# Kernel optimization log

Hardware: AMD Instinct MI355X
Metric: run time of the kernel (lower is better)

The kernel has to match this reference:

```python
import jax, jax.numpy as jnp
import numpy as np


def _conv1d_same(seq, w, b):
    # seq: (N, 1, C), w: (1, 1, K) odd K, bias (1,). SAME padding, stride 1.
    k = w.shape[-1]
    p = (k - 1) // 2
    out = jax.lax.conv_general_dilated(
        seq, w, window_strides=(1,), padding=[(p, p)],
        dimension_numbers=("NCH", "OIH", "NCH"))
    return out + b[None, :, None]


def setup_inputs() -> dict:
    key = jax.random.key(0)
    k1, k2, k3 = jax.random.split(key, 3)
    N, C, H, W = 32, 512, 32, 32
    x = jax.random.normal(k1, (N, C, H, W), dtype=jnp.float32)
    wq = jax.random.normal(k2, (1, 1, 5), dtype=jnp.float32) * 0.2
    bq = jax.random.normal(k3, (1,), dtype=jnp.float32) * 0.1
    return {"x": x, "wq": wq, "bq": bq}


def reference(x, wq, bq):
    N, C, H, W = x.shape
    # Global average pool over spatial dims -> (N, 1, C)
    gap = jnp.mean(x, axis=(2, 3)).reshape(N, 1, C)
    # NOTE: original module applies conv_q to BOTH query and key (conv_k unused)
    query = jax.nn.sigmoid(_conv1d_same(gap, wq, bq))          # (N, 1, C)
    key_t = jnp.transpose(query, (0, 2, 1))                    # (N, C, 1)
    # Outer product key @ query -> (N, C, C), softmax over flattened C*C
    qk = jnp.einsum("nci,nij->ncj", key_t, query)              # (N, C, C)
    qk = jax.nn.softmax(qk.reshape(N, C * C), axis=-1).reshape(N, C, C)
    # value: (N, H*W, C)
    value = jnp.transpose(x, (0, 2, 3, 1)).reshape(N, H * W, C)
    att = jnp.einsum("npc,ncd->npd", value, qk)                # (N, HW, C)
    att = jnp.transpose(att, (0, 2, 1)).reshape(N, C, H, W)
    return x * att
```

## Files before the change

kernel.cpp:

```cpp
#include <hip/hip_runtime.h>
#include <math.h>

#define NB 32
#define CC 512
#define HW 1024
#define NJ 10

__device__ float g_gap[NB * CC];

__device__ __forceinline__ float wave_reduce(float s) {
#pragma unroll
  for (int off = 32; off; off >>= 1) s += __shfl_down(s, off, 64);
  return s;
}

__global__ __launch_bounds__(256) void k_gap(const float* __restrict__ x) {
  int wv = threadIdx.x >> 6, lane = threadIdx.x & 63;
  int r0 = blockIdx.x * 16;
#pragma unroll
  for (int it = 0; it < 4; ++it) {
    int row = r0 + wv * 4 + it;
    const float4* xp = (const float4*)x + (size_t)row * 256;
    float s = 0.f;
#pragma unroll
    for (int k = 0; k < 4; ++k) {
      float4 v = xp[lane + 64 * k];
      s += v.x + v.y + v.z + v.w;
    }
    s = wave_reduce(s);
    if (lane == 0) g_gap[row] = s * (1.0f / 1024.0f);
  }
}

__global__ __launch_bounds__(512) void k_fused(const float* __restrict__ x,
                                               const float* __restrict__ wq,
                                               const float* __restrict__ bq,
                                               float* __restrict__ out) {
  int n = blockIdx.x >> 4, pblk = blockIdx.x & 15;
  int t = threadIdx.x;
  int cg = t >> 4, pg = t & 15;
  int wv = t >> 6, lane = t & 63;

  __shared__ float qs[CC];
  __shared__ float wred[8][NJ];
  __shared__ float4 sred[8][16][NJ + 1];
  __shared__ float4 sfin[16][NJ + 1];
  __shared__ float invZ_sh;

  const float cj[NJ] = {1.f, 1.f, 0.5f, 1.f / 6.f, 1.f / 24.f, 1.f / 120.f,
                        1.f / 720.f, 1.f / 5040.f, 1.f / 40320.f, 1.f / 362880.f};

  float4 xv[16];
  const float4* x4 = (const float4*)x;
  size_t base = (size_t)(n * CC + cg * 16) * 256 + (size_t)pblk * 16 + pg;
#pragma unroll
  for (int i = 0; i < 16; ++i) xv[i] = x4[base + (size_t)i * 256];

  {
    int c = t;
    const float* g = g_gap + n * CC;
    float z = bq[0];
#pragma unroll
    for (int k = 0; k < 5; ++k) {
      int idx = c + k - 2;
      float gv = (idx >= 0 && idx < CC) ? g[idx] : 0.f;
      z = fmaf(gv, wq[k], z);
    }
    float qv = 1.f / (1.f + expf(-z));
    qs[c] = qv;
    float pj[NJ];
    float pw = 1.f;
#pragma unroll
    for (int j = 0; j < NJ; ++j) { pj[j] = pw; pw *= qv; }
#pragma unroll
    for (int j = 0; j < NJ; ++j) pj[j] = wave_reduce(pj[j]);
    if (lane == 0) {
#pragma unroll
      for (int j = 0; j < NJ; ++j) wred[wv][j] = pj[j];
    }
  }
  __syncthreads();
  if (t == 0) {
    float Z = 0.f;
#pragma unroll
    for (int j = 0; j < NJ; ++j) {
      float P = 0.f;
#pragma unroll
      for (int w8 = 0; w8 < 8; ++w8) P += wred[w8][j];
      Z = fmaf(cj[j] * P, P, Z);
    }
    invZ_sh = 1.f / Z;
  }

  float4 acc[NJ];
#pragma unroll
  for (int j = 0; j < NJ; ++j) acc[j] = make_float4(0.f, 0.f, 0.f, 0.f);
#pragma unroll
  for (int i = 0; i < 16; ++i) {
    float qc = qs[cg * 16 + i];
    float4 v = xv[i];
    float w = 1.f;
#pragma unroll
    for (int j = 0; j < NJ; ++j) {
      acc[j].x = fmaf(w, v.x, acc[j].x);
      acc[j].y = fmaf(w, v.y, acc[j].y);
      acc[j].z = fmaf(w, v.z, acc[j].z);
      acc[j].w = fmaf(w, v.w, acc[j].w);
      w *= qc;
    }
  }
#pragma unroll
  for (int j = 0; j < NJ; ++j) {
    acc[j].x += __shfl_xor(acc[j].x, 16, 64);
    acc[j].y += __shfl_xor(acc[j].y, 16, 64);
    acc[j].z += __shfl_xor(acc[j].z, 16, 64);
    acc[j].w += __shfl_xor(acc[j].w, 16, 64);
    acc[j].x += __shfl_xor(acc[j].x, 32, 64);
    acc[j].y += __shfl_xor(acc[j].y, 32, 64);
    acc[j].z += __shfl_xor(acc[j].z, 32, 64);
    acc[j].w += __shfl_xor(acc[j].w, 32, 64);
  }
  if (lane < 16) {
#pragma unroll
    for (int j = 0; j < NJ; ++j) sred[wv][lane][j] = acc[j];
  }
  __syncthreads();
  if (t < 160) {
    int pp = t / NJ, j = t - pp * NJ;
    float4 a = make_float4(0.f, 0.f, 0.f, 0.f);
#pragma unroll
    for (int w8 = 0; w8 < 8; ++w8) {
      float4 v = sred[w8][pp][j];
      a.x += v.x; a.y += v.y; a.z += v.z; a.w += v.w;
    }
    float sc = cj[j] * invZ_sh;
    a.x *= sc; a.y *= sc; a.z *= sc; a.w *= sc;
    sfin[pp][j] = a;
  }
  __syncthreads();

  float4 sj[NJ];
#pragma unroll
  for (int j = 0; j < NJ; ++j) sj[j] = sfin[pg][j];
  float4* o4 = (float4*)out;
#pragma unroll
  for (int i = 0; i < 16; ++i) {
    float qd = qs[cg * 16 + i];
    float w = 1.f;
    float4 att = make_float4(0.f, 0.f, 0.f, 0.f);
#pragma unroll
    for (int j = 0; j < NJ; ++j) {
      att.x = fmaf(w, sj[j].x, att.x);
      att.y = fmaf(w, sj[j].y, att.y);
      att.z = fmaf(w, sj[j].z, att.z);
      att.w = fmaf(w, sj[j].w, att.w);
      w *= qd;
    }
    float4 xvv = xv[i];
    float4 o;
    o.x = xvv.x * att.x; o.y = xvv.y * att.y;
    o.z = xvv.z * att.z; o.w = xvv.w * att.w;
    o4[base + (size_t)i * 256] = o;
  }
}

extern "C" void kernel_launch(void* const* d_in, const int* in_sizes, int n_in,
                              void* d_out, int out_size, void* d_ws, size_t ws_size,
                              hipStream_t stream) {
  const float* x  = (const float*)d_in[0];
  const float* wq = (const float*)d_in[1];
  const float* bq = (const float*)d_in[2];
  float* out = (float*)d_out;
  (void)d_ws; (void)ws_size;

  k_gap<<<NB * CC / 16, 256, 0, stream>>>(x);
  k_fused<<<NB * 16, 512, 0, stream>>>(x, wq, bq, out);
}
```

Baseline: 132.7 us.

## Split query/normalizer into separate kernel and halve per-thread tile in fused kernel

Measured after the change: 143.0 us. +7.8%, slower.

```diff
diff --git a/kernel.cpp b/kernel.cpp
--- a/kernel.cpp
+++ b/kernel.cpp
@@ -6,7 +6,11 @@
 #define HW 1024
 #define NJ 10
 
+typedef float vf4 __attribute__((ext_vector_type(4)));
+
 __device__ float g_gap[NB * CC];
+__device__ float g_q[NB * CC];
+__device__ float g_invZ[NB];
 
 __device__ __forceinline__ float wave_reduce(float s) {
 #pragma unroll
@@ -32,55 +36,37 @@
   }
 }
 
-__global__ __launch_bounds__(512) void k_fused(const float* __restrict__ x,
-                                               const float* __restrict__ wq,
-                                               const float* __restrict__ bq,
-                                               float* __restrict__ out) {
-  int n = blockIdx.x >> 4, pblk = blockIdx.x & 15;
-  int t = threadIdx.x;
-  int cg = t >> 4, pg = t & 15;
-  int wv = t >> 6, lane = t & 63;
-
-  __shared__ float qs[CC];
+__global__ __launch_bounds__(512) void k_q(const float* __restrict__ wq,
+                                           const float* __restrict__ bq) {
+  int n = blockIdx.x, c = threadIdx.x;
+  int wv = c >> 6, lane = c & 63;
+  __shared__ float gsh[CC];
   __shared__ float wred[8][NJ];
-  __shared__ float4 sred[8][16][NJ + 1];
-  __shared__ float4 sfin[16][NJ + 1];
-  __shared__ float invZ_sh;
-
   const float cj[NJ] = {1.f, 1.f, 0.5f, 1.f / 6.f, 1.f / 24.f, 1.f / 120.f,
                         1.f / 720.f, 1.f / 5040.f, 1.f / 40320.f, 1.f / 362880.f};
-
-  float4 xv[16];
-  const float4* x4 = (const float4*)x;
-  size_t base = (size_t)(n * CC + cg * 16) * 256 + (size_t)pblk * 16 + pg;
+  gsh[c] = g_gap[n * CC + c];
+  __syncthreads();
+  float z = bq[0];
 #pragma unroll
-  for (int i = 0; i < 16; ++i) xv[i] = x4[base + (size_t)i * 256];
-
-  {
-    int c = t;
-    const float* g = g_gap + n * CC;
-    float z = bq[0];
+  for (int k = 0; k < 5; ++k) {
+    int idx = c + k - 2;
+    float gv = (idx >= 0 && idx < CC) ? gsh[idx] : 0.f;
+    z = fmaf(gv, wq[k], z);
+  }
+  float qv = 1.f / (1.f + expf(-z));
+  g_q[n * CC + c] = qv;
+  float pj[NJ];
+  float pw = 1.f;
 #pragma unroll
-    for (int k = 0; k < 5; ++k) {
-      int idx = c + k - 2;
-      float gv = (idx >= 0 && idx < CC) ? g[idx] : 0.f;
-      z = fmaf(gv, wq[k], z);
-    }
-    float qv = 1.f / (1.f + expf(-z));
-    qs[c] = qv;
-    float pj[NJ];
-    float pw = 1.f;
+  for (int j = 0; j < NJ; ++j) { pj[j] = pw; pw *= qv; }
 #pragma unroll
-    for (int j = 0; j < NJ; ++j) { pj[j] = pw; pw *= qv; }
+  for (int j = 0; j < NJ; ++j) pj[j] = wave_reduce(pj[j]);
+  if (lane == 0) {
 #pragma unroll
-    for (int j = 0; j < NJ; ++j) pj[j] = wave_reduce(pj[j]);
-    if (lane == 0) {
-#pragma unroll
-      for (int j = 0; j < NJ; ++j) wred[wv][j] = pj[j];
-    }
+    for (int j = 0; j < NJ; ++j) wred[wv][j] = pj[j];
   }
   __syncthreads();
-  if (t == 0) {
+  if (c == 0) {
     float Z = 0.f;
 #pragma unroll
     for (int j = 0; j < NJ; ++j) {
@@ -89,78 +75,94 @@
       for (int w8 = 0; w8 < 8; ++w8) P += wred[w8][j];
       Z = fmaf(cj[j] * P, P, Z);
     }
-    invZ_sh = 1.f / Z;
+    g_invZ[n] = 1.f / Z;
   }
+}
 
-  float4 acc[NJ];
+__global__ __launch_bounds__(512, 2) void k_fused(const float* __restrict__ x,
+                                                  float* __restrict__ out) {
+  int n = blockIdx.x >> 5, pblk = blockIdx.x & 31;
+  int t = threadIdx.x;
+  int cg = t >> 3, pg = t & 7;
+  int wv = t >> 6, lane = t & 63;
+
+  __shared__ vf4 sred[8][8][NJ + 1];
+  __shared__ vf4 sfin[8][NJ + 1];
+
+  const float cj[NJ] = {1.f, 1.f, 0.5f, 1.f / 6.f, 1.f / 24.f, 1.f / 120.f,
+                        1.f / 720.f, 1.f / 5040.f, 1.f / 40320.f, 1.f / 362880.f};
+
+  const vf4* x4 = (const vf4*)x;
+  size_t base = (size_t)(n * CC + cg * 8) * 256 + (size_t)pblk * 8 + pg;
+
+  vf4 xv[8];
 #pragma unroll
-  for (int j = 0; j < NJ; ++j) acc[j] = make_float4(0.f, 0.f, 0.f, 0.f);
+  for (int i = 0; i < 8; ++i)
+    xv[i] = __builtin_nontemporal_load(&x4[base + (size_t)i * 256]);
+
+  float qv8[8];
+  {
+    const vf4* q4 = (const vf4*)g_q;
+    int qi = (n * CC + cg * 8) >> 2;
+    vf4 qa = q4[qi], qb = q4[qi + 1];
+    qv8[0] = qa.x; qv8[1] = qa.y; qv8[2] = qa.z; qv8[3] = qa.w;
+    qv8[4] = qb.x; qv8[5] = qb.y; qv8[6] = qb.z; qv8[7] = qb.w;
+  }
+  float invZ = g_invZ[n];
+
+  vf4 acc[NJ];
 #pragma unroll
-  for (int i = 0; i < 16; ++i) {
-    float qc = qs[cg * 16 + i];
-    float4 v = xv[i];
+  for (int j = 0; j < NJ; ++j) acc[j] = (vf4){0.f, 0.f, 0.f, 0.f};
+#pragma unroll
+  for (int i = 0; i < 8; ++i) {
+    float qc = qv8[i];
+    vf4 v = xv[i];
     float w = 1.f;
 #pragma unroll
     for (int j = 0; j < NJ; ++j) {
-      acc[j].x = fmaf(w, v.x, acc[j].x);
-      acc[j].y = fmaf(w, v.y, acc[j].y);
-      acc[j].z = fmaf(w, v.z, acc[j].z);
-      acc[j].w = fmaf(w, v.w, acc[j].w);
+      acc[j] += v * w;
       w *= qc;
     }
   }
 #pragma unroll
   for (int j = 0; j < NJ; ++j) {
-    acc[j].x += __shfl_xor(acc[j].x, 16, 64);
-    acc[j].y += __shfl_xor(acc[j].y, 16, 64);
-    acc[j].z += __shfl_xor(acc[j].z, 16, 64);
-    acc[j].w += __shfl_xor(acc[j].w, 16, 64);
-    acc[j].x += __shfl_xor(acc[j].x, 32, 64);
-    acc[j].y += __shfl_xor(acc[j].y, 32, 64);
-    acc[j].z += __shfl_xor(acc[j].z, 32, 64);
-    acc[j].w += __shfl_xor(acc[j].w, 32, 64);
+#pragma unroll
+    for (int m = 8; m <= 32; m <<= 1) {
+      acc[j].x += __shfl_xor(acc[j].x, m, 64);
+      acc[j].y += __shfl_xor(acc[j].y, m, 64);
+      acc[j].z += __shfl_xor(acc[j].z, m, 64);
+      acc[j].w += __shfl_xor(acc[j].w, m, 64);
+    }
   }
-  if (lane < 16) {
+  if (lane < 8) {
 #pragma unroll
     for (int j = 0; j < NJ; ++j) sred[wv][lane][j] = acc[j];
   }
   __syncthreads();
-  if (t < 160) {
+  if (t < 80) {
     int pp = t / NJ, j = t - pp * NJ;
-    float4 a = make_float4(0.f, 0.f, 0.f, 0.f);
+    vf4 a = (vf4){0.f, 0.f, 0.f, 0.f};
 #pragma unroll
-    for (int w8 = 0; w8 < 8; ++w8) {
-      float4 v = sred[w8][pp][j];
-      a.x += v.x; a.y += v.y; a.z += v.z; a.w += v.w;
-    }
-    float sc = cj[j] * invZ_sh;
-    a.x *= sc; a.y *= sc; a.z *= sc; a.w *= sc;
-    sfin[pp][j] = a;
+    for (int w8 = 0; w8 < 8; ++w8) a += sred[w8][pp][j];
+    sfin[pp][j] = a * (cj[j] * invZ);
   }
   __syncthreads();
 
-  float4 sj[NJ];
+  vf4 sj[NJ];
 #pragma unroll
   for (int j = 0; j < NJ; ++j) sj[j] = sfin[pg][j];
-  float4* o4 = (float4*)out;
+  vf4* o4 = (vf4*)out;
 #pragma unroll
-  for (int i = 0; i < 16; ++i) {
-    float qd = qs[cg * 16 + i];
+  for (int i = 0; i < 8; ++i) {
+    float qd = qv8[i];
     float w = 1.f;
-    float4 att = make_float4(0.f, 0.f, 0.f, 0.f);
+    vf4 att = (vf4){0.f, 0.f, 0.f, 0.f};
 #pragma unroll
     for (int j = 0; j < NJ; ++j) {
-      att.x = fmaf(w, sj[j].x, att.x);
-      att.y = fmaf(w, sj[j].y, att.y);
-      att.z = fmaf(w, sj[j].z, att.z);
-      att.w = fmaf(w, sj[j].w, att.w);
+      att += sj[j] * w;
       w *= qd;
     }
-    float4 xvv = xv[i];
-    float4 o;
-    o.x = xvv.x * att.x; o.y = xvv.y * att.y;
-    o.z = xvv.z * att.z; o.w = xvv.w * att.w;
-    o4[base + (size_t)i * 256] = o;
+    __builtin_nontemporal_store(xv[i] * att, &o4[base + (size_t)i * 256]);
   }
 }
 
@@ -174,5 +176,6 @@
   (void)d_ws; (void)ws_size;
 
   k_gap<<<NB * CC / 16, 256, 0, stream>>>(x);
-  k_fused<<<NB * 16, 512, 0, stream>>>(x, wq, bq, out);
+  k_q<<<NB, 512, 0, stream>>>(wq, bq);
+  k_fused<<<NB * 32, 512, 0, stream>>>(x, out);
 }
```
